# Kernel tuning notes

Measured on AMD Instinct MI355X. Metric: run time of the kernel, lower is better.

## Reference

```python
import jax, jax.numpy as jnp
import numpy as np

N_NODES = 50000
N_EDGES = 800000
C_IN, C_HID, C_OUT = 256, 128, 64


def gcn_conv(x, src, dst, deg_inv_sqrt, W, b, n_nodes):
    """PyG GCNConv with self-loops already folded into (src, dst, deg).

    out[j] = sum_{(i->j)} d_i^{-1/2} d_j^{-1/2} (x W)[i] + b
    """
    h = x @ W  # [N, out]
    norm = deg_inv_sqrt[src] * deg_inv_sqrt[dst]  # [E+N]
    msg = h[src] * norm[:, None]  # [E+N, out]
    out = jax.ops.segment_sum(msg, dst, num_segments=n_nodes)
    return out + b


def setup_inputs() -> dict:
    key = jax.random.key(0)
    k1, k2, k3, k4, k5, k6 = jax.random.split(key, 6)
    x = jax.random.normal(k1, (N_NODES, C_IN), dtype=jnp.float32)
    edge_index = jax.random.randint(k2, (2, N_EDGES), 0, N_NODES, dtype=jnp.int64)
    # Glorot-ish init for GCN weights
    W1 = jax.random.normal(k3, (C_IN, C_HID), dtype=jnp.float32) / np.sqrt(C_IN)
    b1 = jnp.zeros((C_HID,), dtype=jnp.float32)
    W2 = jax.random.normal(k4, (C_HID, C_OUT), dtype=jnp.float32) / np.sqrt(C_HID)
    b2 = jnp.zeros((C_OUT,), dtype=jnp.float32)
    return {"x": x, "edge_index": edge_index, "W1": W1, "b1": b1, "W2": W2, "b2": b2}


def reference(x, edge_index, W1, b1, W2, b2):
    n = x.shape[0]
    loop = jnp.arange(n, dtype=edge_index.dtype)
    src = jnp.concatenate([edge_index[0], loop])  # row (message source)
    dst = jnp.concatenate([edge_index[1], loop])  # col (aggregation target)
    # symmetric normalization degree: in-degree at dst, with self loops
    deg = jax.ops.segment_sum(jnp.ones_like(dst, dtype=x.dtype), dst, num_segments=n)
    deg_inv_sqrt = jnp.where(deg > 0, jax.lax.rsqrt(deg), 0.0)

    h = gcn_conv(x, src, dst, deg_inv_sqrt, W1, b1, n)
    h = jax.nn.relu(h)
    # Dropout is identity in eval mode (reference baseline is deterministic)
    out = gcn_conv(h, src, dst, deg_inv_sqrt, W2, b2, n)
    return out
```

## Files before the change

kernel.cpp:

```cpp
#include <hip/hip_runtime.h>


#define CIN 256
#define CHID 128
#define COUT 64
#define NSCAT 256

typedef unsigned short ushort_t;
typedef unsigned int uint_t;
typedef __attribute__((ext_vector_type(8))) short short8;
typedef __attribute__((ext_vector_type(4))) float f32x4;

__device__ inline ushort_t f2bf(float f) {
  union { float f; uint_t u; } v; v.f = f;
  uint_t r = v.u + 0x7FFFu + ((v.u >> 16) & 1u);
  return (ushort_t)(r >> 16);
}
__device__ inline float bf_lo(uint_t u) {
  union { uint_t u; float f; } v; v.u = u << 16;
  return v.f;
}
__device__ inline float bf_hi(uint_t u) {
  union { uint_t u; float f; } v; v.u = u & 0xFFFF0000u;
  return v.f;
}
__device__ inline uint_t pack2(float a, float b) {
  return (uint_t)f2bf(a) | ((uint_t)f2bf(b) << 16);
}

__global__ __launch_bounds__(256) void k_pre(const int* __restrict__ dst,
                                             int* __restrict__ cntmat,
                                             const float* __restrict__ W1,
                                             const float* __restrict__ W2,
                                             ushort_t* __restrict__ Wt1,
                                             ushort_t* __restrict__ Wt2,
                                             int e, int nbk) {
  const int tid = threadIdx.x;
  if (blockIdx.x < NSCAT) {
    __shared__ int h[256];
    h[tid] = 0;
    __syncthreads();
    const int per = (e + NSCAT - 1) / NSCAT;
    const int lo = blockIdx.x * per;
    const int hi = min(e, lo + per);
    for (int i = lo + tid; i < hi; i += 256) atomicAdd(&h[dst[i] >> 8], 1);
    __syncthreads();
    if (tid < nbk) cntmat[blockIdx.x * nbk + tid] = h[tid];
  } else {
    int i = (blockIdx.x - NSCAT) * 256 + tid;
    if (i < CIN * CHID) {
      int k = i % CIN, c = i / CIN;
      Wt1[i] = f2bf(W1[(size_t)k * CHID + c]);
    } else {
      int j = i - CIN * CHID;
      if (j < CHID * COUT) {
        int k = j % CHID, c = j / CHID;
        Wt2[j] = f2bf(W2[(size_t)k * COUT + c]);
      }
    }
  }
}

__global__ __launch_bounds__(256) void k_colscan(int* __restrict__ cntmat,
                                                 int* __restrict__ btot, int nbk) {
  __shared__ int s[NSCAT];
  const int k = blockIdx.x;
  const int tid = threadIdx.x;
  const int v = cntmat[tid * nbk + k];
  s[tid] = v;
  __syncthreads();
  for (int off = 1; off < NSCAT; off <<= 1) {
    int t = (tid >= off) ? s[tid - off] : 0;
    __syncthreads();
    s[tid] += t;
    __syncthreads();
  }
  cntmat[tid * nbk + k] = s[tid] - v;
  if (tid == NSCAT - 1) btot[k] = s[tid];
}

__global__ __launch_bounds__(256) void k_bscatter(const int* __restrict__ src,
                                                  const int* __restrict__ dst,
                                                  const int* __restrict__ cntmat,
                                                  const int* __restrict__ btot,
                                                  int* __restrict__ pairs,
                                                  int e, int nbk) {
  __shared__ int s[256];
  __shared__ int cur[256];
  const int tid = threadIdx.x;
  const int v = (tid < nbk) ? btot[tid] : 0;
  s[tid] = v;
  __syncthreads();
  for (int off = 1; off < 256; off <<= 1) {
    int t = (tid >= off) ? s[tid - off] : 0;
    __syncthreads();
    s[tid] += t;
    __syncthreads();
  }
  cur[tid] = (tid < nbk) ? (s[tid] - v + cntmat[blockIdx.x * nbk + tid]) : 0;
  __syncthreads();
  const int per = (e + NSCAT - 1) / NSCAT;
  const int lo = blockIdx.x * per;
  const int hi = min(e, lo + per);
  for (int i = lo + tid; i < hi; i += 256) {
    int d = dst[i];
    int off = atomicAdd(&cur[d >> 8], 1);
    pairs[off] = (src[i] << 8) | (d & 255);
  }
}

__global__ __launch_bounds__(256) void k_bbuild(const int* __restrict__ pairs,
                                                const int* __restrict__ btot,
                                                int* __restrict__ rowptr,
                                                float* __restrict__ dinv,
                                                ushort_t* __restrict__ csr,
                                                int n, int e, int nbk) {
  __shared__ int h[256];
  __shared__ int s[256];
  __shared__ int sbnd[2];
  const int tid = threadIdx.x;
  const int b = blockIdx.x;
  {
    const int v = (tid < nbk) ? btot[tid] : 0;
    s[tid] = v;
    __syncthreads();
    for (int off = 1; off < 256; off <<= 1) {
      int t = (tid >= off) ? s[tid - off] : 0;
      __syncthreads();
      s[tid] += t;
      __syncthreads();
    }
    if (tid == b) {
      sbnd[0] = s[tid] - v;
      sbnd[1] = s[tid];
    }
    __syncthreads();
  }
  const int lo = sbnd[0];
  const int hi = sbnd[1];
  h[tid] = 0;
  __syncthreads();
  for (int i = lo + tid; i < hi; i += 256) atomicAdd(&h[pairs[i] & 255], 1);
  __syncthreads();
  const int deg = h[tid];
  s[tid] = deg;
  __syncthreads();
  for (int off = 1; off < 256; off <<= 1) {
    int t = (tid >= off) ? s[tid - off] : 0;
    __syncthreads();
    s[tid] += t;
    __syncthreads();
  }
  const int excl = s[tid] - deg;
  const int node = (b << 8) + tid;
  if (node < n) {
    rowptr[node] = lo + excl;
    dinv[node] = rsqrtf((float)(deg + 1));
  }
  if (b == 0 && tid == 0) rowptr[n] = e;
  h[tid] = lo + excl;
  __syncthreads();
  for (int i = lo + tid; i < hi; i += 256) {
    int p = pairs[i];
    int slot = atomicAdd(&h[p & 255], 1);
    csr[slot] = (ushort_t)(((uint_t)p) >> 8);
  }
}

template <int K, int BN, int BM, bool XBF16>
__global__ __launch_bounds__(256) void k_gemm_mfma(
    const void* __restrict__ Xv, const ushort_t* __restrict__ Wt,
    const float* __restrict__ dinv, ushort_t* __restrict__ out, int M) {
  constexpr int BK = 32;
  constexpr int MI = BM / 64;
  constexpr int NSUB = BN / 16;
  constexpr int ASZ = BM * BK;
  constexpr int BSZ = BK * BN;
  constexpr int NCH = K / BK;
  constexpr int AIT = ASZ / 8 / 256;
  constexpr int BIT = BSZ / 8 / 256;

  __shared__ ushort_t As[2][ASZ];
  __shared__ ushort_t Bs[2][BSZ];

  const int tid = threadIdx.x;
  const int lane = tid & 63;
  const int w = tid >> 6;
  const int row0 = blockIdx.x * BM;

  const float* Xf = (const float*)Xv;
  const ushort_t* Xb = (const ushort_t*)Xv;

  float4 ar0[AIT], ar1[AIT];
  uint4 arb[AIT];
  uint4 brg[BIT];

  auto load_A = [&](int kc) {
#pragma unroll
    for (int i = 0; i < AIT; ++i) {
      int fi = i * 256 + tid;
      int r = fi % BM, k0 = (fi / BM) * 8;
      int gr = row0 + r;
      if (gr > M - 1) gr = M - 1;
      if (XBF16) {
        arb[i] = *(const uint4*)(Xb + (size_t)gr * K + kc + k0);
      } else {
        ar0[i] = *(const float4*)(Xf + (size_t)gr * K + kc + k0);
        ar1[i] = *(const float4*)(Xf + (size_t)gr * K + kc + k0 + 4);
      }
    }
#pragma unroll
    for (int i = 0; i < BIT; ++i) {
      int g = i * 256 + tid;
      int nf = g >> 6, l = g & 63;
      int c = nf * 16 + (l & 15), k0 = (l >> 4) * 8;
      brg[i] = *(const uint4*)(Wt + (size_t)c * K + kc + k0);
    }
  };

  auto write_lds = [&](int buf) {
#pragma unroll
    for (int i = 0; i < AIT; ++i) {
      int fi = i * 256 + tid;
      int r = fi % BM, kb = fi / BM;
      int flat = (r >> 4) * 512 + ((r & 15) + 16 * kb) * 8;
      if (XBF16) {
        *(uint4*)&As[buf][flat] = arb[i];
      } else {
        uint4 p;
        p.x = pack2(ar0[i].x, ar0[i].y);
        p.y = pack2(ar0[i].z, ar0[i].w);
        p.z = pack2(ar1[i].x, ar1[i].y);
        p.w = pack2(ar1[i].z, ar1[i].w);
        *(uint4*)&As[buf][flat] = p;
      }
    }
#pragma unroll
    for (int i = 0; i < BIT; ++i) {
      int g = i * 256 + tid;
      int nf = g >> 6, l = g & 63;
      *(uint4*)&Bs[buf][nf * 512 + l * 8] = brg[i];
    }
  };

  f32x4 acc[MI][NSUB];
#pragma unroll
  for (int mi = 0; mi < MI; ++mi)
#pragma unroll
    for (int ni = 0; ni < NSUB; ++ni)
      acc[mi][ni] = (f32x4){0.f, 0.f, 0.f, 0.f};

  load_A(0);
  write_lds(0);

#pragma unroll 1
  for (int ch = 0; ch < NCH; ++ch) {
    const int cur = ch & 1;
    __syncthreads();
    if (ch + 1 < NCH) load_A((ch + 1) * BK);

    short8 af[MI];
#pragma unroll
    for (int mi = 0; mi < MI; ++mi)
      af[mi] = *(const short8*)&As[cur][(w * MI + mi) * 512 + lane * 8];
    short8 bf[NSUB];
#pragma unroll
    for (int ni = 0; ni < NSUB; ++ni)
      bf[ni] = *(const short8*)&Bs[cur][ni * 512 + lane * 8];

#pragma unroll
    for (int mi = 0; mi < MI; ++mi)
#pragma unroll
      for (int ni = 0; ni < NSUB; ++ni)
        acc[mi][ni] = __builtin_amdgcn_mfma_f32_16x16x32_bf16(
            af[mi], bf[ni], acc[mi][ni], 0, 0, 0);

    if (ch + 1 < NCH) write_lds(cur ^ 1);
  }

  const int qrow = (lane >> 4) * 4;
  const int col16 = lane & 15;
#pragma unroll
  for (int mi = 0; mi < MI; ++mi) {
    int rbase = row0 + (w * MI + mi) * 16 + qrow;
#pragma unroll
    for (int v = 0; v < 4; ++v) {
      int row = rbase + v;
      if (row < M) {
        float dn = dinv[row];
#pragma unroll
        for (int ni = 0; ni < NSUB; ++ni)
          out[(size_t)row * BN + ni * 16 + col16] = f2bf(dn * acc[mi][ni][v]);
      }
    }
  }
}

__global__ __launch_bounds__(256) void k_aggw_h(
    const ushort_t* __restrict__ hh, const int* __restrict__ rowptr,
    const ushort_t* __restrict__ csr, const float* __restrict__ dinv,
    const float* __restrict__ bias, ushort_t* __restrict__ out, int n) {
  const int tid = threadIdx.x;
  const int node = blockIdx.x * 4 + (tid >> 6);
  if (node >= n) return;
  const int lane = tid & 63;
  const int q = lane & 15;
  const int eg = lane >> 4;

  float acc[8];
#pragma unroll
  for (int j = 0; j < 8; ++j) acc[j] = 0.0f;

  const int beg = rowptr[node];
  const int end = rowptr[node + 1];
  for (int k = beg + eg; k < end; k += 4) {
    int s = csr[k];
    uint4 u = *(const uint4*)&hh[(size_t)s * CHID + q * 8];
    acc[0] += bf_lo(u.x); acc[1] += bf_hi(u.x);
    acc[2] += bf_lo(u.y); acc[3] += bf_hi(u.y);
    acc[4] += bf_lo(u.z); acc[5] += bf_hi(u.z);
    acc[6] += bf_lo(u.w); acc[7] += bf_hi(u.w);
  }
#pragma unroll
  for (int j = 0; j < 8; ++j) {
    acc[j] += __shfl_xor(acc[j], 16);
    acc[j] += __shfl_xor(acc[j], 32);
  }
  if (eg == 0) {
    uint4 u = *(const uint4*)&hh[(size_t)node * CHID + q * 8];
    acc[0] += bf_lo(u.x); acc[1] += bf_hi(u.x);
    acc[2] += bf_lo(u.y); acc[3] += bf_hi(u.y);
    acc[4] += bf_lo(u.z); acc[5] += bf_hi(u.z);
    acc[6] += bf_lo(u.w); acc[7] += bf_hi(u.w);
    const float dn = dinv[node];
    float4 b0 = *(const float4*)&bias[q * 8];
    float4 b1 = *(const float4*)&bias[q * 8 + 4];
    float r[8];
    r[0] = dn * acc[0] + b0.x; r[1] = dn * acc[1] + b0.y;
    r[2] = dn * acc[2] + b0.z; r[3] = dn * acc[3] + b0.w;
    r[4] = dn * acc[4] + b1.x; r[5] = dn * acc[5] + b1.y;
    r[6] = dn * acc[6] + b1.z; r[7] = dn * acc[7] + b1.w;
#pragma unroll
    for (int j = 0; j < 8; ++j) r[j] = fmaxf(r[j], 0.0f);
    uint4 o;
    o.x = pack2(r[0], r[1]); o.y = pack2(r[2], r[3]);
    o.z = pack2(r[4], r[5]); o.w = pack2(r[6], r[7]);
    *(uint4*)&out[(size_t)node * CHID + q * 8] = o;
  }
}

__global__ __launch_bounds__(256) void k_aggw_o(
    const ushort_t* __restrict__ hh, const int* __restrict__ rowptr,
    const ushort_t* __restrict__ csr, const float* __restrict__ dinv,
    const float* __restrict__ bias, float* __restrict__ out, int n) {
  const int tid = threadIdx.x;
  const int node = blockIdx.x * 4 + (tid >> 6);
  if (node >= n) return;
  const int lane = tid & 63;
  const int q = lane & 7;
  const int eg = lane >> 3;

  float acc[8];
#pragma unroll
  for (int j = 0; j < 8; ++j) acc[j] = 0.0f;

  const int beg = rowptr[node];
  const int end = rowptr[node + 1];
  for (int k = beg + eg; k < end; k += 8) {
    int s = csr[k];
    uint4 u = *(const uint4*)&hh[(size_t)s * COUT + q * 8];
    acc[0] += bf_lo(u.x); acc[1] += bf_hi(u.x);
    acc[2] += bf_lo(u.y); acc[3] += bf_hi(u.y);
    acc[4] += bf_lo(u.z); acc[5] += bf_hi(u.z);
    acc[6] += bf_lo(u.w); acc[7] += bf_hi(u.w);
  }
#pragma unroll
  for (int j = 0; j < 8; ++j) {
    acc[j] += __shfl_xor(acc[j], 8);
    acc[j] += __shfl_xor(acc[j], 16);
    acc[j] += __shfl_xor(acc[j], 32);
  }
  if (eg == 0) {
    uint4 u = *(const uint4*)&hh[(size_t)node * COUT + q * 8];
    acc[0] += bf_lo(u.x); acc[1] += bf_hi(u.x);
    acc[2] += bf_lo(u.y); acc[3] += bf_hi(u.y);
    acc[4] += bf_lo(u.z); acc[5] += bf_hi(u.z);
    acc[6] += bf_lo(u.w); acc[7] += bf_hi(u.w);
    const float dn = dinv[node];
    float4 b0 = *(const float4*)&bias[q * 8];
    float4 b1 = *(const float4*)&bias[q * 8 + 4];
    float4 o0, o1;
    o0.x = dn * acc[0] + b0.x; o0.y = dn * acc[1] + b0.y;
    o0.z = dn * acc[2] + b0.z; o0.w = dn * acc[3] + b0.w;
    o1.x = dn * acc[4] + b1.x; o1.y = dn * acc[5] + b1.y;
    o1.z = dn * acc[6] + b1.z; o1.w = dn * acc[7] + b1.w;
    *(float4*)&out[(size_t)node * COUT + q * 8] = o0;
    *(float4*)&out[(size_t)node * COUT + q * 8 + 4] = o1;
  }
}

extern "C" void kernel_launch(void* const* d_in, const int* in_sizes, int n_in,
                              void* d_out, int out_size, void* d_ws, size_t ws_size,
                              hipStream_t stream) {
  const float* x  = (const float*)d_in[0];
  const int*   ei = (const int*)d_in[1];
  const float* W1 = (const float*)d_in[2];
  const float* b1 = (const float*)d_in[3];
  const float* W2 = (const float*)d_in[4];
  const float* b2 = (const float*)d_in[5];
  float* out = (float*)d_out;

  const int n = in_sizes[0] / CIN;
  const int e = in_sizes[1] / 2;
  const int* src = ei;
  const int* dst = ei + e;
  const int nbk = (n + 255) >> 8;

  size_t off = 0;
  auto alloc = [&](size_t bytes) {
    size_t o = off;
    off = (off + bytes + 255) & ~(size_t)255;
    return o;
  };
  char* ws = (char*)d_ws;
  int*      cntmat = (int*)(ws + alloc((size_t)NSCAT * 256 * 4));
  int*      btot   = (int*)(ws + alloc(256 * 4));
  int*      rowptr = (int*)(ws + alloc((size_t)(n + 1) * 4));
  float*    dinv   = (float*)(ws + alloc((size_t)n * 4));
  ushort_t* csr    = (ushort_t*)(ws + alloc((size_t)e * 2));
  int*      pairs  = (int*)(ws + alloc((size_t)e * 4));
  ushort_t* wt1    = (ushort_t*)(ws + alloc((size_t)CIN * CHID * 2));
  ushort_t* wt2    = (ushort_t*)(ws + alloc((size_t)CHID * COUT * 2));
  ushort_t* hhA    = (ushort_t*)(ws + alloc((size_t)n * CHID * 2));
  ushort_t* hhB    = (ushort_t*)(ws + alloc((size_t)n * CHID * 2));

  const int WTB = (CIN * CHID + CHID * COUT + 255) / 256;

  k_pre<<<NSCAT + WTB, 256, 0, stream>>>(dst, cntmat, W1, W2, wt1, wt2, e, nbk);
  k_colscan<<<nbk, NSCAT, 0, stream>>>(cntmat, btot, nbk);
  k_bscatter<<<NSCAT, 256, 0, stream>>>(src, dst, cntmat, btot, pairs, e, nbk);
  k_bbuild<<<nbk, 256, 0, stream>>>(pairs, btot, rowptr, dinv, csr, n, e, nbk);

  k_gemm_mfma<CIN, CHID, 64, false><<<(n + 63) / 64, 256, 0, stream>>>(
      x, wt1, dinv, hhA, n);
  k_aggw_h<<<(n + 3) / 4, 256, 0, stream>>>(hhA, rowptr, csr, dinv, b1, hhB, n);

  k_gemm_mfma<CHID, COUT, 64, true><<<(n + 63) / 64, 256, 0, stream>>>(
      hhB, wt2, dinv, hhA, n);
  k_aggw_o<<<(n + 3) / 4, 256, 0, stream>>>(hhA, rowptr, csr, dinv, b2, out, n);
}
```

Before: 139.6 us.

## Stage full A tile in LDS once and stream weights from global to registers

The GEMM kernel now loads the block's entire 64-row A panel (all of K) into LDS in a single pass with one barrier, replacing the per-chunk double-buffered LDS pipeline that synchronized every K step. The B (weight) fragments are read straight from global memory (likely L2-resident) into registers with a two-deep register prefetch, so B no longer goes through LDS. This removes repeated __syncthreads and LDS traffic for B. In exchange, LDS use grows to 32KB per block for layer 1, which may lower occupancy, and there is no overlap between the A load and compute.

```diff
diff --git a/kernel.cpp b/kernel.cpp
--- a/kernel.cpp
+++ b/kernel.cpp
@@ -167,131 +167,85 @@
   }
 }
 
-template <int K, int BN, int BM, bool XBF16>
-__global__ __launch_bounds__(256) void k_gemm_mfma(
+template <int K, int BN, bool XBF16>
+__global__ __launch_bounds__(256) void k_gemm_os(
     const void* __restrict__ Xv, const ushort_t* __restrict__ Wt,
     const float* __restrict__ dinv, ushort_t* __restrict__ out, int M) {
-  constexpr int BK = 32;
-  constexpr int MI = BM / 64;
+  constexpr int BM = 64, BK = 32;
+  constexpr int NCH = K / BK;
   constexpr int NSUB = BN / 16;
-  constexpr int ASZ = BM * BK;
-  constexpr int BSZ = BK * BN;
-  constexpr int NCH = K / BK;
-  constexpr int AIT = ASZ / 8 / 256;
-  constexpr int BIT = BSZ / 8 / 256;
-
-  __shared__ ushort_t As[2][ASZ];
-  __shared__ ushort_t Bs[2][BSZ];
+
+  __shared__ ushort_t As[BM * K];
 
   const int tid = threadIdx.x;
   const int lane = tid & 63;
   const int w = tid >> 6;
   const int row0 = blockIdx.x * BM;
 
-  const float* Xf = (const float*)Xv;
-  const ushort_t* Xb = (const ushort_t*)Xv;
-
-  float4 ar0[AIT], ar1[AIT];
-  uint4 arb[AIT];
-  uint4 brg[BIT];
-
-  auto load_A = [&](int kc) {
-#pragma unroll
-    for (int i = 0; i < AIT; ++i) {
-      int fi = i * 256 + tid;
-      int r = fi % BM, k0 = (fi / BM) * 8;
-      int gr = row0 + r;
-      if (gr > M - 1) gr = M - 1;
-      if (XBF16) {
-        arb[i] = *(const uint4*)(Xb + (size_t)gr * K + kc + k0);
-      } else {
-        ar0[i] = *(const float4*)(Xf + (size_t)gr * K + kc + k0);
-        ar1[i] = *(const float4*)(Xf + (size_t)gr * K + kc + k0 + 4);
-      }
-    }
-#pragma unroll
-    for (int i = 0; i < BIT; ++i) {
-      int g = i * 256 + tid;
-      int nf = g >> 6, l = g & 63;
-      int c = nf * 16 + (l & 15), k0 = (l >> 4) * 8;
-      brg[i] = *(const uint4*)(Wt + (size_t)c * K + kc + k0);
-    }
-  };
-
-  auto write_lds = [&](int buf) {
-#pragma unroll
-    for (int i = 0; i < AIT; ++i) {
-      int fi = i * 256 + tid;
-      int r = fi % BM, kb = fi / BM;
-      int flat = (r >> 4) * 512 + ((r & 15) + 16 * kb) * 8;
-      if (XBF16) {
-        *(uint4*)&As[buf][flat] = arb[i];
-      } else {
-        uint4 p;
-        p.x = pack2(ar0[i].x, ar0[i].y);
-        p.y = pack2(ar0[i].z, ar0[i].w);
-        p.z = pack2(ar1[i].x, ar1[i].y);
-        p.w = pack2(ar1[i].z, ar1[i].w);
-        *(uint4*)&As[buf][flat] = p;
-      }
-    }
-#pragma unroll
-    for (int i = 0; i < BIT; ++i) {
-      int g = i * 256 + tid;
-      int nf = g >> 6, l = g & 63;
-      *(uint4*)&Bs[buf][nf * 512 + l * 8] = brg[i];
-    }
-  };
-
-  f32x4 acc[MI][NSUB];
-#pragma unroll
-  for (int mi = 0; mi < MI; ++mi)
+#pragma unroll
+  for (int i = 0; i < NCH; ++i) {
+    int fi = i * 256 + tid;
+    int r = fi & 63;
+    int ks = fi >> 6;
+    int kc = ks >> 2, kb = ks & 3;
+    int gr = row0 + r;
+    if (gr > M - 1) gr = M - 1;
+    int flat = ((r >> 4) * NCH + kc) * 512 + ((r & 15) + 16 * kb) * 8;
+    if (XBF16) {
+      *(uint4*)&As[flat] =
+          *(const uint4*)((const ushort_t*)Xv + (size_t)gr * K + ks * 8);
+    } else {
+      const float* Xf = (const float*)Xv;
+      float4 a0 = *(const float4*)(Xf + (size_t)gr * K + ks * 8);
+      float4 a1 = *(const float4*)(Xf + (size_t)gr * K + ks * 8 + 4);
+      uint4 p;
+      p.x = pack2(a0.x, a0.y);
+      p.y = pack2(a0.z, a0.w);
+      p.z = pack2(a1.x, a1.y);
+      p.w = pack2(a1.z, a1.w);
+      *(uint4*)&As[flat] = p;
+    }
+  }
+  __syncthreads();
+
+  const int bcol = lane & 15;
+  const int bk0 = (lane >> 4) * 8;
+  uint4 bfr[2][NSUB];
+
+  f32x4 acc[NSUB];
+#pragma unroll
+  for (int ni = 0; ni < NSUB; ++ni) acc[ni] = (f32x4){0.f, 0.f, 0.f, 0.f};
+
+#pragma unroll
+  for (int ni = 0; ni < NSUB; ++ni)
+    bfr[0][ni] = *(const uint4*)(Wt + (size_t)(ni * 16 + bcol) * K + bk0);
+
+#pragma unroll
+  for (int kc = 0; kc < NCH; ++kc) {
+    if (kc + 1 < NCH) {
+#pragma unroll
+      for (int ni = 0; ni < NSUB; ++ni)
+        bfr[(kc + 1) & 1][ni] = *(const uint4*)(
+            Wt + (size_t)(ni * 16 + bcol) * K + (kc + 1) * BK + bk0);
+    }
+    short8 af = *(const short8*)&As[(w * NCH + kc) * 512 + lane * 8];
 #pragma unroll
     for (int ni = 0; ni < NSUB; ++ni)
-      acc[mi][ni] = (f32x4){0.f, 0.f, 0.f, 0.f};
-
-  load_A(0);
-  write_lds(0);
-
-#pragma unroll 1
-  for (int ch = 0; ch < NCH; ++ch) {
-    const int cur = ch & 1;
-    __syncthreads();
-    if (ch + 1 < NCH) load_A((ch + 1) * BK);
-
-    short8 af[MI];
-#pragma unroll
-    for (int mi = 0; mi < MI; ++mi)
-      af[mi] = *(const short8*)&As[cur][(w * MI + mi) * 512 + lane * 8];
-    short8 bf[NSUB];
-#pragma unroll
-    for (int ni = 0; ni < NSUB; ++ni)
-      bf[ni] = *(const short8*)&Bs[cur][ni * 512 + lane * 8];
-
-#pragma unroll
-    for (int mi = 0; mi < MI; ++mi)
-#pragma unroll
-      for (int ni = 0; ni < NSUB; ++ni)
-        acc[mi][ni] = __builtin_amdgcn_mfma_f32_16x16x32_bf16(
-            af[mi], bf[ni], acc[mi][ni], 0, 0, 0);
-
-    if (ch + 1 < NCH) write_lds(cur ^ 1);
+      acc[ni] = __builtin_amdgcn_mfma_f32_16x16x32_bf16(
+          af, *(const short8*)&bfr[kc & 1][ni], acc[ni], 0, 0, 0);
   }
 
   const int qrow = (lane >> 4) * 4;
   const int col16 = lane & 15;
-#pragma unroll
-  for (int mi = 0; mi < MI; ++mi) {
-    int rbase = row0 + (w * MI + mi) * 16 + qrow;
-#pragma unroll
-    for (int v = 0; v < 4; ++v) {
-      int row = rbase + v;
-      if (row < M) {
-        float dn = dinv[row];
-#pragma unroll
-        for (int ni = 0; ni < NSUB; ++ni)
-          out[(size_t)row * BN + ni * 16 + col16] = f2bf(dn * acc[mi][ni][v]);
-      }
+  const int rbase = row0 + w * 16 + qrow;
+#pragma unroll
+  for (int v = 0; v < 4; ++v) {
+    int row = rbase + v;
+    if (row < M) {
+      float dn = dinv[row];
+#pragma unroll
+      for (int ni = 0; ni < NSUB; ++ni)
+        out[(size_t)row * BN + ni * 16 + col16] = f2bf(dn * acc[ni][v]);
     }
   }
 }
@@ -441,11 +395,11 @@
   k_bscatter<<<NSCAT, 256, 0, stream>>>(src, dst, cntmat, btot, pairs, e, nbk);
   k_bbuild<<<nbk, 256, 0, stream>>>(pairs, btot, rowptr, dinv, csr, n, e, nbk);
 
-  k_gemm_mfma<CIN, CHID, 64, false><<<(n + 63) / 64, 256, 0, stream>>>(
+  k_gemm_os<CIN, CHID, false><<<(n + 63) / 64, 256, 0, stream>>>(
       x, wt1, dinv, hhA, n);
   k_aggw_h<<<(n + 3) / 4, 256, 0, stream>>>(hhA, rowptr, csr, dinv, b1, hhB, n);
 
-  k_gemm_mfma<CHID, COUT, 64, true><<<(n + 63) / 64, 256, 0, stream>>>(
+  k_gemm_os<CHID, COUT, true><<<(n + 63) / 64, 256, 0, stream>>>(
       hhB, wt2, dinv, hhA, n);
   k_aggw_o<<<(n + 3) / 4, 256, 0, stream>>>(hhA, rowptr, csr, dinv, b2, out, n);
 }
```

Result: slower. 154.0 us (+10.3%).
